# Kernel optimization log

Measured on AMD Instinct MI355X. Metric: run time of the kernel, lower is better.

## Reference

```python
import jax, jax.numpy as jnp
import numpy as np

B, C_LOCAL, C_GUIDE, C2, H, W = 16, 256, 256, 256, 64, 64
MID = C2 // 2          # mlp hidden channels
CQ = C_LOCAL // 4      # offset_gen hidden channels (also = groups)
EPS = 1e-5             # BatchNorm eps (inference mode)


def _conv(x, w, pad=0, groups=1, b=None):
    out = jax.lax.conv_general_dilated(
        x, w, window_strides=(1, 1), padding=((pad, pad), (pad, pad)),
        dimension_numbers=('NCHW', 'OIHW', 'NCHW'), feature_group_count=groups)
    if b is not None:
        out = out + b[None, :, None, None]
    return out


def _bn(x, g, b, m, v):
    scale = g / jnp.sqrt(v + EPS)
    return x * scale[None, :, None, None] + (b - m * scale)[None, :, None, None]


def _grid_sample(img, grid):
    # img: [C,H,W]; grid: [H,W,2] with (x,y) in [-1,1]; bilinear, zeros padding,
    # align_corners=False (pixel = ((g+1)*size - 1)/2)
    C, Hh, Ww = img.shape
    ix = (grid[..., 0] + 1.0) * (Ww * 0.5) - 0.5
    iy = (grid[..., 1] + 1.0) * (Hh * 0.5) - 0.5
    x0 = jnp.floor(ix); y0 = jnp.floor(iy)
    x1 = x0 + 1.0;      y1 = y0 + 1.0
    wx1 = ix - x0; wx0 = 1.0 - wx1
    wy1 = iy - y0; wy0 = 1.0 - wy1

    def gather(xi, yi):
        valid = (xi >= 0) & (xi < Ww) & (yi >= 0) & (yi < Hh)
        xc = jnp.clip(xi, 0, Ww - 1).astype(jnp.int32)
        yc = jnp.clip(yi, 0, Hh - 1).astype(jnp.int32)
        return img[:, yc, xc] * valid.astype(img.dtype)[None]  # [C,H,W]

    return (gather(x0, y0) * (wx0 * wy0)[None]
            + gather(x1, y0) * (wx1 * wy0)[None]
            + gather(x0, y1) * (wx0 * wy1)[None]
            + gather(x1, y1) * (wx1 * wy1)[None])


def setup_inputs() -> dict:
    key = jax.random.key(0)
    ks = jax.random.split(key, 20)
    w = lambda k, s: jax.random.normal(k, s, jnp.float32) * 0.05
    return {
        'x_local': jax.random.normal(ks[0], (B, C_LOCAL, H, W), jnp.float32),
        'x_guide': jax.random.normal(ks[1], (B, C_GUIDE, H, W), jnp.float32),
        'w_align': w(ks[2], (C2, C_GUIDE, 1, 1)),
        'bn1_g': 1.0 + 0.1 * jax.random.normal(ks[3], (C2,), jnp.float32),
        'bn1_b': 0.1 * jax.random.normal(ks[4], (C2,), jnp.float32),
        'bn1_m': 0.1 * jax.random.normal(ks[5], (C2,), jnp.float32),
        'bn1_v': 0.5 + jax.random.uniform(ks[6], (C2,), jnp.float32),
        'w_off1': w(ks[7], (CQ, 4, 3, 3)),   # grouped: in-ch per group = C_LOCAL/CQ = 4
        'w_off2': w(ks[8], (2, CQ, 1, 1)),
        'b_off2': 0.1 * jax.random.normal(ks[9], (2,), jnp.float32),
        'w_mlp1': w(ks[10], (MID, C_LOCAL, 1, 1)),
        'bn2_g': 1.0 + 0.1 * jax.random.normal(ks[11], (MID,), jnp.float32),
        'bn2_b': 0.1 * jax.random.normal(ks[12], (MID,), jnp.float32),
        'bn2_m': 0.1 * jax.random.normal(ks[13], (MID,), jnp.float32),
        'bn2_v': 0.5 + jax.random.uniform(ks[14], (MID,), jnp.float32),
        'w_mlp2': w(ks[15], (C2, MID, 1, 1)),
    }


def reference(x_local, x_guide, w_align, bn1_g, bn1_b, bn1_m, bn1_v,
              w_off1, w_off2, b_off2, w_mlp1, bn2_g, bn2_b, bn2_m, bn2_v,
              w_mlp2):
    # align(x_guide): 1x1 conv + BN
    g = _bn(_conv(x_guide, w_align), bn1_g, bn1_b, bn1_m, bn1_v)
    # offset_gen(x_local): grouped 3x3 conv -> SiLU -> 1x1 conv (bias) -> [B,2,H,W]
    off = _conv(x_local, w_off1, pad=1, groups=CQ)
    off = _conv(jax.nn.silu(off), w_off2, b=b_off2)
    # base grid in [-1,1], (x,y) last
    ys = jnp.linspace(-1.0, 1.0, H)
    xs = jnp.linspace(-1.0, 1.0, W)
    gy, gx = jnp.meshgrid(ys, xs, indexing='ij')
    base = jnp.stack((gx, gy), axis=-1)                      # [H,W,2]
    v_grid = base[None] + off.transpose(0, 2, 3, 1) * (2.0 / max(H, W))
    g_aligned = jax.vmap(_grid_sample)(g, v_grid)            # [B,C2,H,W]
    # mlp(x_local): 1x1 conv -> BN -> GELU(exact) -> 1x1 conv
    l = _conv(x_local, w_mlp1)
    l = jax.nn.gelu(_bn(l, bn2_g, bn2_b, bn2_m, bn2_v), approximate=False)
    l = _conv(l, w_mlp2)
    return jax.nn.silu(g_aligned + l)
```

## Files before the change

### kernel.cpp

```cpp
#include <hip/hip_runtime.h>

typedef unsigned short u16;
typedef unsigned int u32;
typedef __bf16 bf16x8 __attribute__((ext_vector_type(8)));
typedef float f32x4 __attribute__((ext_vector_type(4)));
typedef u16 u16x4 __attribute__((ext_vector_type(4)));
typedef u16 u16x8 __attribute__((ext_vector_type(8)));

#define EPS 1e-5f

__device__ __forceinline__ u16 f2bf(float f) {
  unsigned u = __builtin_bit_cast(unsigned, f);
  u += 0x7FFFu + ((u >> 16) & 1u);
  return (u16)(u >> 16);
}
__device__ __forceinline__ float bf2f(u16 h) {
  unsigned u = ((unsigned)h) << 16;
  return __builtin_bit_cast(float, u);
}

__global__ void prep_weights(
    const float* __restrict__ wa, const float* __restrict__ g1, const float* __restrict__ b1,
    const float* __restrict__ m1, const float* __restrict__ v1,
    const float* __restrict__ w1, const float* __restrict__ g2, const float* __restrict__ b2,
    const float* __restrict__ m2, const float* __restrict__ v2,
    const float* __restrict__ w2,
    u16* __restrict__ Acat, u16* __restrict__ w1_o,
    float* __restrict__ bias1, float* __restrict__ bias2) {
  int c = blockIdx.x, k = threadIdx.x;
  float s1 = g1[c] / sqrtf(v1[c] + EPS);
  if (k < 256) Acat[c * 384 + k] = f2bf(wa[c * 256 + k] * s1);
  else         Acat[c * 384 + k] = f2bf(w2[c * 128 + (k - 256)]);
  if (c < 128) {
    float s2 = g2[c] / sqrtf(v2[c] + EPS);
    if (k < 256) w1_o[c * 256 + k] = f2bf(w1[c * 256 + k] * s2);
    if (k == 256) bias2[c] = b2[c] - m2[c] * s2;
  }
  if (k == 0) bias1[c] = b1[c] - m1[c] * s1;
}

__global__ __launch_bounds__(256) void gconv_kernel(
    const float* __restrict__ xl, const float* __restrict__ w1,
    u16* __restrict__ sbuf) {
  __shared__ float tile[4][18][68];
  const int tid = threadIdx.x;
  const int band = blockIdx.x;
  const int q = blockIdx.y;
  const int b = blockIdx.z;
  const float* xb = xl + ((size_t)b * 256 + 4 * q) * 4096;

  if (tid < 72) {
    int ci0 = tid / 18, r0_ = tid - ci0 * 18;
    float* rowp = &tile[ci0][r0_][0];
    rowp[0] = 0.f; rowp[65] = 0.f; rowp[66] = 0.f; rowp[67] = 0.f;
  }

  const int ci = tid >> 6, col = tid & 63;
  const int gy0 = band * 16 - 1;
  const float* cp = xb + (size_t)ci * 4096 + col;
  float v[18];
#pragma unroll
  for (int r = 0; r < 18; ++r) {
    int gy = gy0 + r;
    int gyc = min(max(gy, 0), 63);
    float raw = cp[gyc * 64];
    v[r] = ((unsigned)gy < 64u) ? raw : 0.f;
  }
#pragma unroll
  for (int r = 0; r < 18; ++r) tile[ci][r][col + 1] = v[r];

  float wq[36];
#pragma unroll
  for (int i = 0; i < 36; ++i) wq[i] = w1[q * 36 + i];
  __syncthreads();

  const int qx = tid & 15, ry = tid >> 4;
  float a0 = 0.f, a1 = 0.f, a2 = 0.f, a3 = 0.f;
#pragma unroll
  for (int ci2 = 0; ci2 < 4; ++ci2) {
#pragma unroll
    for (int dy = 0; dy < 3; ++dy) {
      const float* rowp = &tile[ci2][ry + dy][qx * 4];
      f32x4 m = *(const f32x4*)rowp;
      float2 e = *(const float2*)(rowp + 4);
      float w0 = wq[ci2 * 9 + dy * 3 + 0];
      float w1_ = wq[ci2 * 9 + dy * 3 + 1];
      float w2_ = wq[ci2 * 9 + dy * 3 + 2];
      a0 += w0 * m[0] + w1_ * m[1] + w2_ * m[2];
      a1 += w0 * m[1] + w1_ * m[2] + w2_ * m[3];
      a2 += w0 * m[2] + w1_ * m[3] + w2_ * e.x;
      a3 += w0 * m[3] + w1_ * e.x  + w2_ * e.y;
    }
  }
  u16x4 o;
  o[0] = f2bf(a0 / (1.f + __expf(-a0)));
  o[1] = f2bf(a1 / (1.f + __expf(-a1)));
  o[2] = f2bf(a2 / (1.f + __expf(-a2)));
  o[3] = f2bf(a3 / (1.f + __expf(-a3)));
  u16* sp = sbuf + ((size_t)(b * 64 + q)) * 4096 + (band * 16 + ry) * 64 + qx * 4;
  *(u16x4*)sp = o;
}

__global__ __launch_bounds__(256) void coords_kernel(
    const u16* __restrict__ sbuf, const float* __restrict__ w2,
    const float* __restrict__ b2, float* __restrict__ coords,
    float* __restrict__ wsum) {
  __shared__ float sw2[128];
  const int tid = threadIdx.x;
  if (tid < 128) sw2[tid] = w2[tid];
  __syncthreads();
  const int b = blockIdx.y;
  const int p = blockIdx.x * 256 + tid;
  const u16* sp = sbuf + (size_t)b * 64 * 4096 + p;
  float ax = 0.f, ay = 0.f;
#pragma unroll 8
  for (int q = 0; q < 64; ++q) {
    float v = bf2f(sp[(size_t)q * 4096]);
    ax += sw2[q] * v;
    ay += sw2[64 + q] * v;
  }
  int y = p >> 6, x = p & 63;
  float ix = (64.f / 63.f) * (float)x + ax + b2[0] - 0.5f;
  float iy = (64.f / 63.f) * (float)y + ay + b2[1] - 0.5f;
  ((float2*)coords)[(size_t)b * 4096 + p] = make_float2(ix, iy);
  float x0f = floorf(ix), y0f = floorf(iy);
  int x0 = (int)x0f, y0 = (int)y0f;
  float wx1 = ix - x0f, wx0 = 1.f - wx1;
  float wy1 = iy - y0f, wy0 = 1.f - wy1;
  bool vx0 = (unsigned)x0 < 64u, vx1 = (unsigned)(x0 + 1) < 64u;
  bool vy0 = (unsigned)y0 < 64u, vy1 = (unsigned)(y0 + 1) < 64u;
  float s = (vx0 && vy0 ? wx0 * wy0 : 0.f) + (vx1 && vy0 ? wx1 * wy0 : 0.f) +
            (vx0 && vy1 ? wx0 * wy1 : 0.f) + (vx1 && vy1 ? wx1 * wy1 : 0.f);
  wsum[(size_t)b * 4096 + p] = s;
}

__global__ __launch_bounds__(256, 1) void sampler_kernel(
    const float* __restrict__ xg, const float* __restrict__ coords,
    u16* __restrict__ xh) {
  __shared__ u16 t[64 * 72];
  const int wg = blockIdx.x;
  const int id = (wg & 7) * 512 + (wg >> 3);
  const int kq = id >> 10;
  const int b = (id >> 6) & 15, row = id & 63;
  const int tid = threadIdx.x;
  const int px = tid & 63, ko = tid >> 6;
  const int p = row * 64 + px;
  float2 cd = ((const float2*)coords)[(size_t)b * 4096 + p];
  float ix = cd.x, iy = cd.y;
  float x0f = floorf(ix), y0f = floorf(iy);
  int x0 = (int)x0f, y0 = (int)y0f;
  float wx1 = ix - x0f, wx0 = 1.f - wx1;
  float wy1 = iy - y0f, wy0 = 1.f - wy1;
  bool vx0 = (unsigned)x0 < 64u, vx1 = (unsigned)(x0 + 1) < 64u;
  bool vy0 = (unsigned)y0 < 64u, vy1 = (unsigned)(y0 + 1) < 64u;
  int x0c = min(max(x0, 0), 63), x1c = min(max(x0 + 1, 0), 63);
  int y0c = min(max(y0, 0), 63), y1c = min(max(y0 + 1, 0), 63);
  float w00 = (vx0 && vy0) ? wx0 * wy0 : 0.f;
  float w10 = (vx1 && vy0) ? wx1 * wy0 : 0.f;
  float w01 = (vx0 && vy1) ? wx0 * wy1 : 0.f;
  float w11 = (vx1 && vy1) ? wx1 * wy1 : 0.f;
  const int xb2 = min(max(x0, 0), 62);
  const bool sel0 = (x0c != xb2);
  const bool sel1 = (x1c != xb2);
  const int i0t = y0c * 64 + xb2;
  const int i0b = y1c * 64 + xb2;
  const float* bb = xg + ((size_t)b * 256 + kq * 64 + ko * 16) * 4096;

  float2 ft[16], fb_[16];
#pragma unroll
  for (int kk = 0; kk < 16; ++kk) {
    const float* bp = bb + (size_t)kk * 4096;
    ft[kk] = *(const float2*)(bp + i0t);
    fb_[kk] = *(const float2*)(bp + i0b);
  }
  u16 o[16];
#pragma unroll
  for (int kk = 0; kk < 16; ++kk) {
    float v00 = sel0 ? ft[kk].y : ft[kk].x;
    float v10 = sel1 ? ft[kk].y : ft[kk].x;
    float v01 = sel0 ? fb_[kk].y : fb_[kk].x;
    float v11 = sel1 ? fb_[kk].y : fb_[kk].x;
    float v = w00 * v00 + w10 * v10 + w01 * v01 + w11 * v11;
    o[kk] = f2bf(v);
  }
  *(u16x8*)&t[px * 72 + ko * 16] = *(u16x8*)&o[0];
  *(u16x8*)&t[px * 72 + ko * 16 + 8] = *(u16x8*)&o[8];
  __syncthreads();
  const int seg = tid & 7, pxa = tid >> 3;
  u16* base = xh + ((size_t)b * 4096 + row * 64) * 384 + kq * 64 + seg * 8;
#pragma unroll
  for (int h = 0; h < 2; ++h) {
    int pp = pxa + h * 32;
    *(u16x8*)(base + (size_t)pp * 384) = *(const u16x8*)&t[pp * 72 + seg * 8];
  }
}

__global__ __launch_bounds__(256, 2) void gemm_h(
    const u16* __restrict__ A, const float* __restrict__ Bsrc,
    u16* __restrict__ xh, const float* __restrict__ bias) {
  __shared__ u16 Al[2][128][40];
  __shared__ u16 Bl[2][128][40];
  const int tid = threadIdx.x;
  const int b = blockIdx.y;
  const int n0 = blockIdx.x * 128;
  const int wave = tid >> 6, lane = tid & 63;
  const int wr = wave >> 1, wc = wave & 1;
  const int lr = lane & 15, kg = lane >> 4;
  f32x4 acc[4][4] = {};
  const float* Bf = Bsrc + (size_t)b * 256 * 4096;

  const int am = tid >> 1, apos = (tid & 1) * 16;
  const int nq = tid & 31, kq = tid >> 5;
  const int nb = n0 + nq * 4;

  u16x8 qa0, qa1;
  f32x4 qb[4];
  {
    qa0 = *(const u16x8*)(A + (size_t)am * 256 + 0 + apos);
    qa1 = *(const u16x8*)(A + (size_t)am * 256 + 0 + apos + 8);
#pragma unroll
    for (int i = 0; i < 4; ++i)
      qb[i] = *(const f32x4*)(Bf + (size_t)(kq * 4 + i) * 4096 + nb);
  }
  int cur = 0;
  for (int kt = 0; kt < 8; ++kt) {
    *(u16x8*)&Al[cur][am][apos] = qa0;
    *(u16x8*)&Al[cur][am][apos + 8] = qa1;
#pragma unroll
    for (int j = 0; j < 4; ++j) {
      u16x4 w = {f2bf(qb[0][j]), f2bf(qb[1][j]), f2bf(qb[2][j]), f2bf(qb[3][j])};
      *(u16x4*)&Bl[cur][nq * 4 + j][kq * 4] = w;
    }
    if (kt < 7) {
      int k1 = (kt + 1) * 32;
      qa0 = *(const u16x8*)(A + (size_t)am * 256 + k1 + apos);
      qa1 = *(const u16x8*)(A + (size_t)am * 256 + k1 + apos + 8);
#pragma unroll
      for (int i = 0; i < 4; ++i)
        qb[i] = *(const f32x4*)(Bf + (size_t)(k1 + kq * 4 + i) * 4096 + nb);
    }
    __syncthreads();
    bf16x8 af[4], bfr[4];
#pragma unroll
    for (int i = 0; i < 4; ++i) {
      af[i] = *(const bf16x8*)&Al[cur][wr * 64 + i * 16 + lr][kg * 8];
      bfr[i] = *(const bf16x8*)&Bl[cur][wc * 64 + i * 16 + lr][kg * 8];
    }
#pragma unroll
    for (int i = 0; i < 4; ++i)
#pragma unroll
      for (int j = 0; j < 4; ++j)
        acc[i][j] = __builtin_amdgcn_mfma_f32_16x16x32_bf16(af[i], bfr[j], acc[i][j], 0, 0, 0);
    cur ^= 1;
  }
  u16* O = xh + (size_t)b * 4096 * 384 + 256;
#pragma unroll
  for (int i = 0; i < 4; ++i) {
    int rb = wr * 64 + i * 16 + kg * 4;
    f32x4 b4 = *(const f32x4*)(bias + rb);
#pragma unroll
    for (int j = 0; j < 4; ++j) {
      int col = n0 + wc * 64 + j * 16 + lr;
      u16x4 w;
#pragma unroll
      for (int e = 0; e < 4; ++e) {
        float v = acc[i][j][e] + b4[e];
        v = 0.5f * v * (1.f + erff(v * 0.70710678118f));
        w[e] = f2bf(v);
      }
      *(u16x4*)(O + (size_t)col * 384 + rb) = w;
    }
  }
}

__global__ __launch_bounds__(256) void gemm_final(
    const u16* __restrict__ A,
    const u16* __restrict__ xh,
    const float* __restrict__ bias1, const float* __restrict__ wsum,
    float* __restrict__ out) {
  __shared__ __attribute__((aligned(16))) u16 Al[2][128][40];
  __shared__ u16 Bl[2][128][40];
  const int tid = threadIdx.x;
  const int wg = blockIdx.y * 64 + blockIdx.x;
  const int nmb = (wg & 7) * 128 + (wg >> 3);
  const int m = nmb & 1;
  const int n0 = ((nmb >> 1) & 31) * 128;
  const int b = nmb >> 6;
  const int wave = tid >> 6, lane = tid & 63;
  const int wr = wave >> 1, wc = wave & 1;
  const int lr = lane & 15, kg = lane >> 4;
  f32x4 acc[4][4] = {};
  const u16* Ab = A + (size_t)m * 128 * 384;
  const u16* Bb = xh + ((size_t)b * 4096 + n0) * 384;

  const int r0 = tid >> 2, pos0 = (tid & 3) * 8;
  const int r1 = (tid + 256) >> 2, pos1 = pos0;

  u16x8 pa0, pa1, pb0, pb1;
  {
    pa0 = *(const u16x8*)(Ab + (size_t)r0 * 384 + 0 + pos0);
    pb0 = *(const u16x8*)(Bb + (size_t)r0 * 384 + 0 + pos0);
    pa1 = *(const u16x8*)(Ab + (size_t)r1 * 384 + 0 + pos1);
    pb1 = *(const u16x8*)(Bb + (size_t)r1 * 384 + 0 + pos1);
  }
  int cur = 0;
  for (int kt = 0; kt < 12; ++kt) {
    *(u16x8*)&Al[cur][r0][pos0] = pa0;
    *(u16x8*)&Bl[cur][r0][pos0] = pb0;
    *(u16x8*)&Al[cur][r1][pos1] = pa1;
    *(u16x8*)&Bl[cur][r1][pos1] = pb1;
    if (kt < 11) {
      int k1 = (kt + 1) * 32;
      pa0 = *(const u16x8*)(Ab + (size_t)r0 * 384 + k1 + pos0);
      pb0 = *(const u16x8*)(Bb + (size_t)r0 * 384 + k1 + pos0);
      pa1 = *(const u16x8*)(Ab + (size_t)r1 * 384 + k1 + pos1);
      pb1 = *(const u16x8*)(Bb + (size_t)r1 * 384 + k1 + pos1);
    }
    __syncthreads();
    bf16x8 af[4], bfr[4];
#pragma unroll
    for (int i = 0; i < 4; ++i) {
      af[i] = *(const bf16x8*)&Al[cur][wr * 64 + i * 16 + lr][kg * 8];
      bfr[i] = *(const bf16x8*)&Bl[cur][wc * 64 + i * 16 + lr][kg * 8];
    }
#pragma unroll
    for (int i = 0; i < 4; ++i)
#pragma unroll
      for (int j = 0; j < 4; ++j)
        acc[i][j] = __builtin_amdgcn_mfma_f32_16x16x32_bf16(af[i], bfr[j], acc[i][j], 0, 0, 0);
    cur ^= 1;
  }

  float* rep = (float*)&Al[0][0][0];
  float* Ob = out + (size_t)b * 256 * 4096;
  float wsv[4];
#pragma unroll
  for (int j = 0; j < 4; ++j)
    wsv[j] = wsum[(size_t)b * 4096 + n0 + wc * 64 + j * 16 + lr];

#pragma unroll
  for (int i = 0; i < 4; ++i) {
    __syncthreads();
    f32x4 b4 = *(const f32x4*)(bias1 + m * 128 + wr * 64 + i * 16 + kg * 4);
#pragma unroll
    for (int j = 0; j < 4; ++j) {
#pragma unroll
      for (int e = 0; e < 4; ++e) {
        float v = acc[i][j][e] + b4[e] * wsv[j];
        v = v / (1.f + __expf(-v));
        rep[(wr * 16 + kg * 4 + e) * 132 + wc * 64 + j * 16 + lr] = v;
      }
    }
    __syncthreads();
#pragma unroll
    for (int pass = 0; pass < 4; ++pass) {
      int lr_ = pass * 8 + (tid >> 5);
      int lc_ = (tid & 31) * 4;
      f32x4 v4 = *(const f32x4*)&rep[lr_ * 132 + lc_];
      int grow = m * 128 + (lr_ >> 4) * 64 + i * 16 + (lr_ & 15);
      *(f32x4*)&Ob[(size_t)grow * 4096 + n0 + lc_] = v4;
    }
  }
}

extern "C" void kernel_launch(void* const* d_in, const int* in_sizes, int n_in,
                              void* d_out, int out_size, void* d_ws, size_t ws_size,
                              hipStream_t stream) {
  const float* x_local = (const float*)d_in[0];
  const float* x_guide = (const float*)d_in[1];
  const float* w_align = (const float*)d_in[2];
  const float* bn1_g = (const float*)d_in[3];
  const float* bn1_b = (const float*)d_in[4];
  const float* bn1_m = (const float*)d_in[5];
  const float* bn1_v = (const float*)d_in[6];
  const float* w_off1 = (const float*)d_in[7];
  const float* w_off2 = (const float*)d_in[8];
  const float* b_off2 = (const float*)d_in[9];
  const float* w_mlp1 = (const float*)d_in[10];
  const float* bn2_g = (const float*)d_in[11];
  const float* bn2_b = (const float*)d_in[12];
  const float* bn2_m = (const float*)d_in[13];
  const float* bn2_v = (const float*)d_in[14];
  const float* w_mlp2 = (const float*)d_in[15];

  char* ws = (char*)d_ws;
  u16* Acat = (u16*)(ws + 0);
  u16* w1_bf = (u16*)(ws + 196608);
  float* bias1 = (float*)(ws + 262144);
  float* bias2 = (float*)(ws + 263168);
  float* wsum = (float*)(ws + 263680);
  float* coords = (float*)(ws + 525824);
  u16* xh = (u16*)(ws + 1050112);
  u16* sbuf = (u16*)d_out;

  prep_weights<<<256, 384, 0, stream>>>(
      w_align, bn1_g, bn1_b, bn1_m, bn1_v,
      w_mlp1, bn2_g, bn2_b, bn2_m, bn2_v, w_mlp2,
      Acat, w1_bf, bias1, bias2);

  gconv_kernel<<<dim3(4, 64, 16), 256, 0, stream>>>(x_local, w_off1, sbuf);

  coords_kernel<<<dim3(16, 16), 256, 0, stream>>>(sbuf, w_off2, b_off2, coords, wsum);

  sampler_kernel<<<4096, 256, 0, stream>>>(x_guide, coords, xh);

  gemm_h<<<dim3(32, 16), 256, 0, stream>>>(w1_bf, x_local, xh, bias2);

  gemm_final<<<dim3(64, 16), 256, 0, stream>>>(Acat, xh, bias1, wsum, (float*)d_out);
}
```

Before: 107.6 us.

## Merge sampler and mlp1 GEMM into one heterogeneous kernel launch

Combines the grid-sample kernel and the first MLP GEMM (with bias and GELU) into a single launch of 4608 blocks. In each group of nine blocks, slot 4 runs a GEMM tile and the other eight run sampler rows. The aim is to overlap the gather-bound sampler with the MFMA-bound GEMM and to remove one launch and its tail. The GEMM path drops its LDS double buffer for a single buffer with two barriers per k-step, which adds synchronization and exposes load latency. It also runs at the sampler's launch bound of one block per SIMD group, lower than the GEMM's previous occupancy.

```diff
diff --git a/kernel.cpp b/kernel.cpp
--- a/kernel.cpp
+++ b/kernel.cpp
@@ -134,141 +134,144 @@
   wsum[(size_t)b * 4096 + p] = s;
 }
 
-__global__ __launch_bounds__(256, 1) void sampler_kernel(
+__global__ __launch_bounds__(256, 1) void fat2_kernel(
     const float* __restrict__ xg, const float* __restrict__ coords,
-    u16* __restrict__ xh) {
-  __shared__ u16 t[64 * 72];
-  const int wg = blockIdx.x;
-  const int id = (wg & 7) * 512 + (wg >> 3);
-  const int kq = id >> 10;
-  const int b = (id >> 6) & 15, row = id & 63;
+    u16* __restrict__ xh,
+    const u16* __restrict__ A, const float* __restrict__ xl,
+    const float* __restrict__ bias) {
+  __shared__ __attribute__((aligned(16))) char lds[20480];
   const int tid = threadIdx.x;
-  const int px = tid & 63, ko = tid >> 6;
-  const int p = row * 64 + px;
-  float2 cd = ((const float2*)coords)[(size_t)b * 4096 + p];
-  float ix = cd.x, iy = cd.y;
-  float x0f = floorf(ix), y0f = floorf(iy);
-  int x0 = (int)x0f, y0 = (int)y0f;
-  float wx1 = ix - x0f, wx0 = 1.f - wx1;
-  float wy1 = iy - y0f, wy0 = 1.f - wy1;
-  bool vx0 = (unsigned)x0 < 64u, vx1 = (unsigned)(x0 + 1) < 64u;
-  bool vy0 = (unsigned)y0 < 64u, vy1 = (unsigned)(y0 + 1) < 64u;
-  int x0c = min(max(x0, 0), 63), x1c = min(max(x0 + 1, 0), 63);
-  int y0c = min(max(y0, 0), 63), y1c = min(max(y0 + 1, 0), 63);
-  float w00 = (vx0 && vy0) ? wx0 * wy0 : 0.f;
-  float w10 = (vx1 && vy0) ? wx1 * wy0 : 0.f;
-  float w01 = (vx0 && vy1) ? wx0 * wy1 : 0.f;
-  float w11 = (vx1 && vy1) ? wx1 * wy1 : 0.f;
-  const int xb2 = min(max(x0, 0), 62);
-  const bool sel0 = (x0c != xb2);
-  const bool sel1 = (x1c != xb2);
-  const int i0t = y0c * 64 + xb2;
-  const int i0b = y1c * 64 + xb2;
-  const float* bb = xg + ((size_t)b * 256 + kq * 64 + ko * 16) * 4096;
-
-  float2 ft[16], fb_[16];
-#pragma unroll
-  for (int kk = 0; kk < 16; ++kk) {
-    const float* bp = bb + (size_t)kk * 4096;
-    ft[kk] = *(const float2*)(bp + i0t);
-    fb_[kk] = *(const float2*)(bp + i0b);
-  }
-  u16 o[16];
-#pragma unroll
-  for (int kk = 0; kk < 16; ++kk) {
-    float v00 = sel0 ? ft[kk].y : ft[kk].x;
-    float v10 = sel1 ? ft[kk].y : ft[kk].x;
-    float v01 = sel0 ? fb_[kk].y : fb_[kk].x;
-    float v11 = sel1 ? fb_[kk].y : fb_[kk].x;
-    float v = w00 * v00 + w10 * v10 + w01 * v01 + w11 * v11;
-    o[kk] = f2bf(v);
-  }
-  *(u16x8*)&t[px * 72 + ko * 16] = *(u16x8*)&o[0];
-  *(u16x8*)&t[px * 72 + ko * 16 + 8] = *(u16x8*)&o[8];
-  __syncthreads();
-  const int seg = tid & 7, pxa = tid >> 3;
-  u16* base = xh + ((size_t)b * 4096 + row * 64) * 384 + kq * 64 + seg * 8;
-#pragma unroll
-  for (int h = 0; h < 2; ++h) {
-    int pp = pxa + h * 32;
-    *(u16x8*)(base + (size_t)pp * 384) = *(const u16x8*)&t[pp * 72 + seg * 8];
-  }
-}
-
-__global__ __launch_bounds__(256, 2) void gemm_h(
-    const u16* __restrict__ A, const float* __restrict__ Bsrc,
-    u16* __restrict__ xh, const float* __restrict__ bias) {
-  __shared__ u16 Al[2][128][40];
-  __shared__ u16 Bl[2][128][40];
-  const int tid = threadIdx.x;
-  const int b = blockIdx.y;
-  const int n0 = blockIdx.x * 128;
-  const int wave = tid >> 6, lane = tid & 63;
-  const int wr = wave >> 1, wc = wave & 1;
-  const int lr = lane & 15, kg = lane >> 4;
-  f32x4 acc[4][4] = {};
-  const float* Bf = Bsrc + (size_t)b * 256 * 4096;
-
-  const int am = tid >> 1, apos = (tid & 1) * 16;
-  const int nq = tid & 31, kq = tid >> 5;
-  const int nb = n0 + nq * 4;
-
-  u16x8 qa0, qa1;
-  f32x4 qb[4];
-  {
-    qa0 = *(const u16x8*)(A + (size_t)am * 256 + 0 + apos);
-    qa1 = *(const u16x8*)(A + (size_t)am * 256 + 0 + apos + 8);
-#pragma unroll
-    for (int i = 0; i < 4; ++i)
-      qb[i] = *(const f32x4*)(Bf + (size_t)(kq * 4 + i) * 4096 + nb);
-  }
-  int cur = 0;
-  for (int kt = 0; kt < 8; ++kt) {
-    *(u16x8*)&Al[cur][am][apos] = qa0;
-    *(u16x8*)&Al[cur][am][apos + 8] = qa1;
-#pragma unroll
-    for (int j = 0; j < 4; ++j) {
-      u16x4 w = {f2bf(qb[0][j]), f2bf(qb[1][j]), f2bf(qb[2][j]), f2bf(qb[3][j])};
-      *(u16x4*)&Bl[cur][nq * 4 + j][kq * 4] = w;
-    }
-    if (kt < 7) {
-      int k1 = (kt + 1) * 32;
-      qa0 = *(const u16x8*)(A + (size_t)am * 256 + k1 + apos);
-      qa1 = *(const u16x8*)(A + (size_t)am * 256 + k1 + apos + 8);
+  const int bid = blockIdx.x;
+  const int grp = bid / 9;
+  const int slot = bid - grp * 9;
+
+  if (slot == 4) {
+    u16 (*Al)[40] = (u16(*)[40])lds;
+    u16 (*Bl)[40] = (u16(*)[40])(lds + 10240);
+    const int b = grp >> 5;
+    const int n0 = (grp & 31) * 128;
+    const int wave = tid >> 6, lane = tid & 63;
+    const int wr = wave >> 1, wc = wave & 1;
+    const int lr = lane & 15, kg = lane >> 4;
+    f32x4 acc[4][4] = {};
+    const float* Bf = xl + (size_t)b * 256 * 4096;
+
+    const int am = tid >> 1, apos = (tid & 1) * 16;
+    const int nq = tid & 31, kq = tid >> 5;
+    const int nb = n0 + nq * 4;
+
+    u16x8 qa0, qa1;
+    f32x4 qb[4];
+    {
+      qa0 = *(const u16x8*)(A + (size_t)am * 256 + 0 + apos);
+      qa1 = *(const u16x8*)(A + (size_t)am * 256 + 0 + apos + 8);
 #pragma unroll
       for (int i = 0; i < 4; ++i)
-        qb[i] = *(const f32x4*)(Bf + (size_t)(k1 + kq * 4 + i) * 4096 + nb);
-    }
+        qb[i] = *(const f32x4*)(Bf + (size_t)(kq * 4 + i) * 4096 + nb);
+    }
+    for (int kt = 0; kt < 8; ++kt) {
+      *(u16x8*)&Al[am][apos] = qa0;
+      *(u16x8*)&Al[am][apos + 8] = qa1;
+#pragma unroll
+      for (int j = 0; j < 4; ++j) {
+        u16x4 w = {f2bf(qb[0][j]), f2bf(qb[1][j]), f2bf(qb[2][j]), f2bf(qb[3][j])};
+        *(u16x4*)&Bl[nq * 4 + j][kq * 4] = w;
+      }
+      if (kt < 7) {
+        int k1 = (kt + 1) * 32;
+        qa0 = *(const u16x8*)(A + (size_t)am * 256 + k1 + apos);
+        qa1 = *(const u16x8*)(A + (size_t)am * 256 + k1 + apos + 8);
+#pragma unroll
+        for (int i = 0; i < 4; ++i)
+          qb[i] = *(const f32x4*)(Bf + (size_t)(k1 + kq * 4 + i) * 4096 + nb);
+      }
+      __syncthreads();
+      bf16x8 af[4], bfr[4];
+#pragma unroll
+      for (int i = 0; i < 4; ++i) {
+        af[i] = *(const bf16x8*)&Al[wr * 64 + i * 16 + lr][kg * 8];
+        bfr[i] = *(const bf16x8*)&Bl[wc * 64 + i * 16 + lr][kg * 8];
+      }
+#pragma unroll
+      for (int i = 0; i < 4; ++i)
+#pragma unroll
+        for (int j = 0; j < 4; ++j)
+          acc[i][j] = __builtin_amdgcn_mfma_f32_16x16x32_bf16(af[i], bfr[j], acc[i][j], 0, 0, 0);
+      __syncthreads();
+    }
+    u16* O = xh + (size_t)b * 4096 * 384 + 256;
+#pragma unroll
+    for (int i = 0; i < 4; ++i) {
+      int rb = wr * 64 + i * 16 + kg * 4;
+      f32x4 b4 = *(const f32x4*)(bias + rb);
+#pragma unroll
+      for (int j = 0; j < 4; ++j) {
+        int col = n0 + wc * 64 + j * 16 + lr;
+        u16x4 w;
+#pragma unroll
+        for (int e = 0; e < 4; ++e) {
+          float v = acc[i][j][e] + b4[e];
+          v = 0.5f * v * (1.f + erff(v * 0.70710678118f));
+          w[e] = f2bf(v);
+        }
+        *(u16x4*)(O + (size_t)col * 384 + rb) = w;
+      }
+    }
+  } else {
+    u16* t = (u16*)lds;
+    const int idx = grp * 8 + (slot < 4 ? slot : slot - 1);
+    const int id = (idx & 7) * 512 + (idx >> 3);
+    const int kq = id >> 10;
+    const int b = (id >> 6) & 15, row = id & 63;
+    const int px = tid & 63, ko = tid >> 6;
+    const int p = row * 64 + px;
+    float2 cd = ((const float2*)coords)[(size_t)b * 4096 + p];
+    float ix = cd.x, iy = cd.y;
+    float x0f = floorf(ix), y0f = floorf(iy);
+    int x0 = (int)x0f, y0 = (int)y0f;
+    float wx1 = ix - x0f, wx0 = 1.f - wx1;
+    float wy1 = iy - y0f, wy0 = 1.f - wy1;
+    bool vx0 = (unsigned)x0 < 64u, vx1 = (unsigned)(x0 + 1) < 64u;
+    bool vy0 = (unsigned)y0 < 64u, vy1 = (unsigned)(y0 + 1) < 64u;
+    int x0c = min(max(x0, 0), 63), x1c = min(max(x0 + 1, 0), 63);
+    int y0c = min(max(y0, 0), 63), y1c = min(max(y0 + 1, 0), 63);
+    float w00 = (vx0 && vy0) ? wx0 * wy0 : 0.f;
+    float w10 = (vx1 && vy0) ? wx1 * wy0 : 0.f;
+    float w01 = (vx0 && vy1) ? wx0 * wy1 : 0.f;
+    float w11 = (vx1 && vy1) ? wx1 * wy1 : 0.f;
+    const int xb2 = min(max(x0, 0), 62);
+    const bool sel0 = (x0c != xb2);
+    const bool sel1 = (x1c != xb2);
+    const int i0t = y0c * 64 + xb2;
+    const int i0b = y1c * 64 + xb2;
+    const float* bb = xg + ((size_t)b * 256 + kq * 64 + ko * 16) * 4096;
+
+    float2 ft[16], fb_[16];
+#pragma unroll
+    for (int kk = 0; kk < 16; ++kk) {
+      const float* bp = bb + (size_t)kk * 4096;
+      ft[kk] = *(const float2*)(bp + i0t);
+      fb_[kk] = *(const float2*)(bp + i0b);
+    }
+    u16 o[16];
+#pragma unroll
+    for (int kk = 0; kk < 16; ++kk) {
+      float v00 = sel0 ? ft[kk].y : ft[kk].x;
+      float v10 = sel1 ? ft[kk].y : ft[kk].x;
+      float v01 = sel0 ? fb_[kk].y : fb_[kk].x;
+      float v11 = sel1 ? fb_[kk].y : fb_[kk].x;
+      float v = w00 * v00 + w10 * v10 + w01 * v01 + w11 * v11;
+      o[kk] = f2bf(v);
+    }
+    *(u16x8*)&t[px * 72 + ko * 16] = *(u16x8*)&o[0];
+    *(u16x8*)&t[px * 72 + ko * 16 + 8] = *(u16x8*)&o[8];
     __syncthreads();
-    bf16x8 af[4], bfr[4];
-#pragma unroll
-    for (int i = 0; i < 4; ++i) {
-      af[i] = *(const bf16x8*)&Al[cur][wr * 64 + i * 16 + lr][kg * 8];
-      bfr[i] = *(const bf16x8*)&Bl[cur][wc * 64 + i * 16 + lr][kg * 8];
-    }
-#pragma unroll
-    for (int i = 0; i < 4; ++i)
-#pragma unroll
-      for (int j = 0; j < 4; ++j)
-        acc[i][j] = __builtin_amdgcn_mfma_f32_16x16x32_bf16(af[i], bfr[j], acc[i][j], 0, 0, 0);
-    cur ^= 1;
-  }
-  u16* O = xh + (size_t)b * 4096 * 384 + 256;
-#pragma unroll
-  for (int i = 0; i < 4; ++i) {
-    int rb = wr * 64 + i * 16 + kg * 4;
-    f32x4 b4 = *(const f32x4*)(bias + rb);
-#pragma unroll
-    for (int j = 0; j < 4; ++j) {
-      int col = n0 + wc * 64 + j * 16 + lr;
-      u16x4 w;
-#pragma unroll
-      for (int e = 0; e < 4; ++e) {
-        float v = acc[i][j][e] + b4[e];
-        v = 0.5f * v * (1.f + erff(v * 0.70710678118f));
-        w[e] = f2bf(v);
-      }
-      *(u16x4*)(O + (size_t)col * 384 + rb) = w;
+    const int seg = tid & 7, pxa = tid >> 3;
+    u16* base = xh + ((size_t)b * 4096 + row * 64) * 384 + kq * 64 + seg * 8;
+#pragma unroll
+    for (int h = 0; h < 2; ++h) {
+      int pp = pxa + h * 32;
+      *(u16x8*)(base + (size_t)pp * 384) = *(const u16x8*)&t[pp * 72 + seg * 8];
     }
   }
 }
@@ -402,9 +405,8 @@
 
   coords_kernel<<<dim3(16, 16), 256, 0, stream>>>(sbuf, w_off2, b_off2, coords, wsum);
 
-  sampler_kernel<<<4096, 256, 0, stream>>>(x_guide, coords, xh);
-
-  gemm_h<<<dim3(32, 16), 256, 0, stream>>>(w1_bf, x_local, xh, bias2);
+  fat2_kernel<<<4608, 256, 0, stream>>>(
+      x_guide, coords, xh, w1_bf, x_local, bias2);
 
   gemm_final<<<dim3(64, 16), 256, 0, stream>>>(Acat, xh, bias1, wsum, (float*)d_out);
 }
```

Result: slower. 116.4 us (+8.2%).
